# Optimization experiments

Hardware: AMD Instinct MI355X
Metric: run time of the kernel (lower is better)

The kernel has to match this reference:

```python
import jax, jax.numpy as jnp
import numpy as np

WINDOW_SIZE = 2
SOFTMAX_TEMP = 0.01
EPS = 1e-12  # F.normalize default eps


def _l2_normalize(x, axis):
    n = jnp.sqrt(jnp.sum(x * x, axis=axis, keepdims=True))
    return x / jnp.maximum(n, EPS)


def setup_inputs() -> dict:
    key = jax.random.key(0)
    k1, k2, k3 = jax.random.split(key, 3)
    B, C, N = 16, 128, 4096
    return {
        "keypoint_coords": jax.random.normal(k1, (B, 2, N), dtype=jnp.float32),
        "keypoint_weights": jax.random.uniform(k2, (B, 1, N), dtype=jnp.float32),
        "keypoint_desc": jax.random.normal(k3, (B, C, N), dtype=jnp.float32),
    }


def reference(keypoint_coords, keypoint_weights, keypoint_desc):
    # split interleaved src/tgt frames along batch
    src_coords = keypoint_coords[::WINDOW_SIZE]    # [b,2,N]
    tgt_coords = keypoint_coords[1::WINDOW_SIZE]   # [b,2,M]
    src_weights = keypoint_weights[::WINDOW_SIZE]  # [b,1,N]
    tgt_weights = keypoint_weights[1::WINDOW_SIZE] # [b,1,M]
    src_desc = keypoint_desc[::WINDOW_SIZE]        # [b,C,N]
    tgt_desc = keypoint_desc[1::WINDOW_SIZE]       # [b,C,M]

    C = src_desc.shape[1]
    src_desc_norm = _l2_normalize(src_desc, axis=1)
    tgt_desc_norm = _l2_normalize(tgt_desc, axis=1)

    # cosine similarity matrix [b,N,M]
    match_vals = jnp.einsum("bcn,bcm->bnm", src_desc_norm, tgt_desc_norm)
    soft_match_vals = jax.nn.softmax(match_vals / SOFTMAX_TEMP, axis=2)

    # reuse the attention matrix for three value matmuls
    pseudo_coords = jnp.einsum("bcm,bnm->bcn", tgt_coords, soft_match_vals)   # [b,2,N]
    pseudo_desc = jnp.einsum("bcm,bnm->bcn", tgt_desc, soft_match_vals)       # [b,C,N]
    pseudo_desc = _l2_normalize(pseudo_desc, axis=1)
    pseudo_weights = jnp.einsum("bim,bnm->bin", tgt_weights, soft_match_vals) # [b,1,N]

    desc_match_score = jnp.sum(src_desc * pseudo_desc, axis=1, keepdims=True) / float(C)
    match_weights = 0.5 * (desc_match_score + 1.0) * src_weights * pseudo_weights
    return pseudo_coords, match_weights
```

## Files before the change

kernel.cpp:

```cpp
#include <hip/hip_runtime.h>
#include <math.h>

#define C 128
#define N 4096
#define BP 8
#define TN 64

typedef __attribute__((ext_vector_type(8))) short bf16x8;
typedef __attribute__((ext_vector_type(16))) float f32x16;
typedef __attribute__((ext_vector_type(4))) int i32x4;
typedef __attribute__((ext_vector_type(16))) int i32x16;

#define PREP_OFF 65536
#define FRAGS_PER_MT 18
#define SUBT_BYTES (FRAGS_PER_MT * 1024)
#define BLOB_BYTES ((size_t)BP * 128 * FRAGS_PER_MT * 1024)

__device__ __forceinline__ unsigned short bf16rnd(float x) {
  unsigned u = __float_as_uint(x);
  u += 0x7fffu + ((u >> 16) & 1u);
  return (unsigned short)(u >> 16);
}
__device__ __forceinline__ float bf16up(unsigned short h) {
  return __uint_as_float(((unsigned)h) << 16);
}
__device__ __forceinline__ int rne2(float x, float y) {
  unsigned ux = __float_as_uint(x); ux += 0x7fffu + ((ux >> 16) & 1u);
  unsigned uy = __float_as_uint(y); uy += 0x7fffu + ((uy >> 16) & 1u);
  return (int)__builtin_amdgcn_perm(uy, ux, 0x07060302u);
}
__device__ __forceinline__ int trunc2(float x, float y) {
  return (int)__builtin_amdgcn_perm(__float_as_uint(y), __float_as_uint(x), 0x07060302u);
}
__device__ __forceinline__ float truncres(float x) {
  return x - __uint_as_float(__float_as_uint(x) & 0xffff0000u);
}
__device__ __forceinline__ int pk4(int a, int b, int c, int d) {
  return (a & 255) | ((b & 255) << 8) | ((c & 255) << 16) | ((d & 255) << 24);
}

__global__ __launch_bounds__(256) void knorm_inv(const float* __restrict__ desc,
                                                 float* __restrict__ inv) {
  int n = blockIdx.x * 256 + threadIdx.x;
  int b = 2 * blockIdx.y + 1;
  const float* d = desc + (size_t)b * C * N + n;
  float ssq = 0.f;
#pragma unroll 8
  for (int c = 0; c < C; ++c) {
    float v = d[(size_t)c * N];
    ssq = fmaf(v, v, ssq);
  }
  inv[b * N + n] = 1.0f / fmaxf(sqrtf(ssq), 1e-12f);
}

__global__ __launch_bounds__(256) void kprep(
    const float* __restrict__ coords, const float* __restrict__ wtsp,
    const float* __restrict__ desc, unsigned char* __restrict__ blob) {
  const int mt = blockIdx.x;
  const int p = blockIdx.y;
  const int tb = 2 * p + 1;
  const int m0 = mt * 32;
  const int t = threadIdx.x;
  const int ks = t >> 6;
  const int h = (t >> 5) & 1;
  const int l31 = t & 31;

  __shared__ float rss[8][32];

  const float* tgtd = desc + (size_t)tb * C * N;
  unsigned char* bl = blob + ((size_t)(p * 128 + mt) * FRAGS_PER_MT) * 1024;

  float vr[16];
  float part = 0.f;
#pragma unroll
  for (int i = 0; i < 16; ++i) {
    float v = tgtd[(size_t)(32 * ks + 16 * h + i) * N + m0 + l31];
    vr[i] = v;
    part = fmaf(v, v, part);
  }
  rss[ks * 2 + h][l31] = part;
  __syncthreads();
  float ssq = 0.f;
#pragma unroll
  for (int u = 0; u < 8; ++u) ssq += rss[u][l31];
  const float invm = 1.0f / fmaxf(sqrtf(ssq), 1e-12f);

  {
    int hb[16], lb[16];
#pragma unroll
    for (int i = 0; i < 16; ++i) {
      int q = (int)rintf(vr[i] * invm * 16384.f);
      int hi = (q + 128) >> 8;
      hb[i] = hi;
      lb[i] = q - (hi << 8);
    }
    int4 ph = make_int4(pk4(hb[0], hb[1], hb[2], hb[3]), pk4(hb[4], hb[5], hb[6], hb[7]),
                        pk4(hb[8], hb[9], hb[10], hb[11]), pk4(hb[12], hb[13], hb[14], hb[15]));
    int4 pl = make_int4(pk4(lb[0], lb[1], lb[2], lb[3]), pk4(lb[4], lb[5], lb[6], lb[7]),
                        pk4(lb[8], lb[9], lb[10], lb[11]), pk4(lb[12], lb[13], lb[14], lb[15]));
    int lane = 32 * h + l31;
    *(int4*)(bl + (size_t)ks * 1024 + lane * 16) = ph;
    *(int4*)(bl + (size_t)(4 + ks) * 1024 + lane * 16) = pl;
  }

#pragma unroll
  for (int it = 0; it < 4; ++it) {
    int e = t + 256 * it;
    int c = e >> 3, mq = e & 7;
    float4 v = *(const float4*)&tgtd[(size_t)c * N + m0 + 4 * mq];
    int f = (c >> 5) * 2 + (mq >> 2);
    int slot = (c & 31) + 32 * ((mq >> 1) & 1);
    int2 pk;
    pk.x = rne2(v.x, v.y);
    pk.y = rne2(v.z, v.w);
    *(int2*)(bl + (size_t)(8 + f) * 1024 + slot * 16 + (mq & 1) * 8) = pk;
  }

  if (t < 128) {
    int fe = t >> 6, slot = t & 63, r = slot & 31, hh = slot >> 5;
    int4 pk = make_int4(0, 0, 0, 0);
    if (r < 4) {
      const float* rp = (r == 0)   ? coords + (size_t)tb * 2 * N
                        : (r == 1) ? coords + (size_t)tb * 2 * N + N
                                   : wtsp + (size_t)tb * N;
      int mb = m0 + 16 * fe + 8 * hh;
      float v[8];
#pragma unroll
      for (int i = 0; i < 8; ++i) v[i] = (r == 3) ? 1.0f : rp[mb + i];
      pk.x = rne2(v[0], v[1]);
      pk.y = rne2(v[2], v[3]);
      pk.z = rne2(v[4], v[5]);
      pk.w = rne2(v[6], v[7]);
    }
    *(int4*)(bl + (size_t)(16 + fe) * 1024 + slot * 16) = pk;
  }
}

#define LDS_SHORTS 32768

__global__ __launch_bounds__(256, 2) void kmain(
    const float* __restrict__ wtsp, const float* __restrict__ desc,
    const unsigned char* __restrict__ blob, float* __restrict__ out) {
  const int bid = blockIdx.x;
  const int p = bid & 7;
  const int ntile = bid >> 3;
  const int sb = 2 * p;
  const int n0 = ntile * TN;
  const int tid = threadIdx.x;
  const int w = tid >> 6;
  const int ln = tid & 63;
  const int l31 = ln & 31;
  const int h = ln >> 5;
  const int wn = w & 1;
  const int st = w >> 1;

  __shared__ __align__(16) short L[LDS_SHORTS];

  const float* srcd = desc + (size_t)sb * C * N;
  const unsigned char* wblob = blob + (size_t)p * 128 * SUBT_BYTES;
  const int nn = n0 + 32 * wn + l31;

  float ssq = 0.f;
#pragma unroll
  for (int ks = 0; ks < 4; ++ks) {
#pragma unroll
    for (int i = 0; i < 16; ++i) {
      float v = srcd[(size_t)(32 * ks + 16 * h + i) * N + nn];
      ssq = fmaf(v, v, ssq);
    }
  }
  ssq += __shfl_xor(ssq, 32);
  const float invs = 1.0f / fmaxf(sqrtf(ssq), 1e-12f);

  i32x4 Qhi[4], Qlo[4];
#pragma unroll
  for (int ks = 0; ks < 4; ++ks) {
    int hb[16], lb[16];
#pragma unroll
    for (int i = 0; i < 16; ++i) {
      float v = srcd[(size_t)(32 * ks + 16 * h + i) * N + nn] * invs;
      int q = (int)rintf(v * 16384.f);
      int hi = (q + 128) >> 8;
      hb[i] = hi;
      lb[i] = q - (hi << 8);
    }
    i32x4 qh = {pk4(hb[0], hb[1], hb[2], hb[3]), pk4(hb[4], hb[5], hb[6], hb[7]),
                pk4(hb[8], hb[9], hb[10], hb[11]), pk4(hb[12], hb[13], hb[14], hb[15])};
    i32x4 ql = {pk4(lb[0], lb[1], lb[2], lb[3]), pk4(lb[4], lb[5], lb[6], lb[7]),
                pk4(lb[8], lb[9], lb[10], lb[11]), pk4(lb[12], lb[13], lb[14], lb[15])};
    Qhi[ks] = qh;
    Qlo[ks] = ql;
  }

  f32x16 acc[5];
#pragma unroll
  for (int t = 0; t < 5; ++t)
#pragma unroll
    for (int r = 0; r < 16; ++r) acc[t][r] = 0.f;

  i32x16 zz;
#pragma unroll
  for (int r = 0; r < 16; ++r) zz[r] = 0;

  auto issue_dma = [&](int it) {
    const unsigned char* s0 = wblob + (size_t)(it * 2) * SUBT_BYTES + ln * 16;
    short* dst = &L[(it & 3) * 8192];
#pragma unroll
    for (int jj = 0; jj < 4; ++jj) {
      int jg = 4 * w + jj;
      const unsigned char* src = s0 + (size_t)(jg >> 3) * SUBT_BYTES + (size_t)(jg & 7) * 1024;
      __builtin_amdgcn_global_load_lds(
          (const void __attribute__((address_space(1)))*)src,
          (void __attribute__((address_space(3)))*)&dst[jg * 512], 16, 0, 0);
    }
  };
  auto loadV = [&](int it2, int s2, bf16x8* V) {
    const unsigned char* vb =
        wblob + (size_t)(it2 * 2 + st) * SUBT_BYTES + (size_t)(8 + s2) * 1024 + ln * 16;
#pragma unroll
    for (int t = 0; t < 5; ++t) V[t] = *(const bf16x8*)(vb + (size_t)(2 * t) * 1024);
  };

  bf16x8 V0[5], V1[5];

  auto compute_iter = [&](int it) {
    const short* vb = &L[(it & 3) * 8192 + st * 4096];

    i32x16 Shh, Sx, Sll;
    {
      i32x4 ah = *(const i32x4*)&vb[0 * 512 + ln * 8];
      i32x4 al = *(const i32x4*)&vb[4 * 512 + ln * 8];
      Shh = __builtin_amdgcn_mfma_i32_32x32x32_i8(ah, Qhi[0], zz, 0, 0, 0);
      Sx = __builtin_amdgcn_mfma_i32_32x32x32_i8(ah, Qlo[0], zz, 0, 0, 0);
      Sll = __builtin_amdgcn_mfma_i32_32x32x32_i8(al, Qlo[0], zz, 0, 0, 0);
      Sx = __builtin_amdgcn_mfma_i32_32x32x32_i8(al, Qhi[0], Sx, 0, 0, 0);
    }
#pragma unroll
    for (int ks = 1; ks < 4; ++ks) {
      i32x4 ah = *(const i32x4*)&vb[ks * 512 + ln * 8];
      i32x4 al = *(const i32x4*)&vb[(4 + ks) * 512 + ln * 8];
      Shh = __builtin_amdgcn_mfma_i32_32x32x32_i8(ah, Qhi[ks], Shh, 0, 0, 0);
      Sx = __builtin_amdgcn_mfma_i32_32x32x32_i8(ah, Qlo[ks], Sx, 0, 0, 0);
      Sll = __builtin_amdgcn_mfma_i32_32x32x32_i8(al, Qlo[ks], Sll, 0, 0, 0);
      Sx = __builtin_amdgcn_mfma_i32_32x32x32_i8(al, Qhi[ks], Sx, 0, 0, 0);
    }

    loadV(it, 1, V1);

    int pp[8], xpp[8];
#pragma unroll
    for (int q = 0; q < 4; ++q) {
      float pv[4];
#pragma unroll
      for (int j = 0; j < 4; ++j) {
        int r = 4 * q + j;
        int tot = (Shh[r] << 8) + Sx[r];
        float sf = fmaf((float)tot, 256.f, (float)Sll[r]);
        pv[j] = __expf(fmaf(sf, 3.7252903e-07f, -60.0f));
      }
      pp[2 * q] = rne2(pv[0], pv[1]);
      pp[2 * q + 1] = rne2(pv[2], pv[3]);
    }
#pragma unroll
    for (int j = 0; j < 8; ++j) xpp[j] = __shfl_xor(pp[j], 32);

    {
      int4 bi;
      if (h == 0)
        bi = make_int4(pp[0], pp[1], xpp[0], xpp[1]);
      else
        bi = make_int4(xpp[2], xpp[3], pp[2], pp[3]);
      bf16x8 bh = __builtin_bit_cast(bf16x8, bi);
#pragma unroll
      for (int t = 0; t < 5; ++t)
        acc[t] = __builtin_amdgcn_mfma_f32_32x32x16_bf16(V0[t], bh, acc[t], 0, 0, 0);
    }

    {
      int itn = (it < 63) ? it + 1 : 63;
      loadV(itn, 0, V0);
    }

    {
      int4 bi;
      if (h == 0)
        bi = make_int4(pp[4], pp[5], xpp[4], xpp[5]);
      else
        bi = make_int4(xpp[6], xpp[7], pp[6], pp[7]);
      bf16x8 bh = __builtin_bit_cast(bf16x8, bi);
#pragma unroll
      for (int t = 0; t < 5; ++t)
        acc[t] = __builtin_amdgcn_mfma_f32_32x32x16_bf16(V1[t], bh, acc[t], 0, 0, 0);
    }
  };

  issue_dma(0);
  issue_dma(1);
  loadV(0, 0, V0);
  __syncthreads();

  for (int it2 = 0; it2 < 32; ++it2) {
    if (it2 < 31) {
      issue_dma(2 * it2 + 2);
      issue_dma(2 * it2 + 3);
    }
    compute_iter(2 * it2);
    compute_iter(2 * it2 + 1);
    __syncthreads();
  }

  float* red = (float*)&L[0];
  if (st == 1) {
#pragma unroll
    for (int t = 0; t < 5; ++t)
#pragma unroll
      for (int r = 0; r < 16; ++r)
        red[wn * 5120 + t * 1024 + r * 64 + ln] = acc[t][r];
  }
  __syncthreads();

  if (st == 0) {
#pragma unroll
    for (int t = 0; t < 5; ++t)
#pragma unroll
      for (int r = 0; r < 16; ++r)
        acc[t][r] += red[wn * 5120 + t * 1024 + r * 64 + ln];

    float ssqd = 0.f, dotr = 0.f;
#pragma unroll
    for (int t = 0; t < 4; ++t) {
#pragma unroll
      for (int r = 0; r < 16; ++r) {
        int c = 32 * t + (r & 3) + 8 * (r >> 2) + 4 * h;
        float d = acc[t][r];
        ssqd = fmaf(d, d, ssqd);
        dotr = fmaf(d, srcd[(size_t)c * N + nn], dotr);
      }
    }
    ssqd += __shfl_xor(ssqd, 32);
    dotr += __shfl_xor(dotr, 32);
    if (h == 0) {
      float x = acc[4][0], y = acc[4][1], wv = acc[4][2], Ld = acc[4][3];
      float invL = 1.0f / Ld;
      float nrm = fmaxf(sqrtf(ssqd), 1e-30f);
      float score = dotr / (nrm * 128.0f);
      float sw = wtsp[(size_t)sb * N + nn];
      out[(size_t)p * 2 * N + nn] = x * invL;
      out[(size_t)p * 2 * N + N + nn] = y * invL;
      out[(size_t)(BP * 2 * N) + (size_t)p * N + nn] =
          0.5f * (score + 1.0f) * sw * wv * invL;
    }
  }
}

#define OFF_VMH3 0
#define OFF_VML3 8192
#define OFF_VCM3 16384
#define OFF_PH3 26624
#define LDS3_SHORTS 30720

__global__ __launch_bounds__(256, 2) void kmain_v3(
    const float* __restrict__ coords, const float* __restrict__ wtsp,
    const float* __restrict__ desc, const float* __restrict__ inv,
    float* __restrict__ out) {
  const int ntile = blockIdx.x;
  const int p = blockIdx.y;
  const int sb = 2 * p, tb = 2 * p + 1;
  const int n0 = ntile * TN;
  const int tid = threadIdx.x;
  const int w = tid >> 6;
  const int ln = tid & 63;
  const int l31 = ln & 31;
  const int h = ln >> 5;
  const int wn = w & 1;
  const int st = w >> 1;
  const int pt = wn * 64 + ln;

  __shared__ __align__(16) short L[LDS3_SHORTS];

  const float* srcd = desc + (size_t)sb * C * N;
  const float* tgtd = desc + (size_t)tb * C * N;
  const float* invtg = inv + tb * N;
  const float* tcx = coords + (size_t)tb * 2 * N;
  const float* tcy = tcx + N;
  const float* twp = wtsp + (size_t)tb * N;
  const int nn = n0 + 32 * wn + l31;

  float ssq = 0.f;
#pragma unroll
  for (int k = 0; k < 8; ++k) {
    int cb = 16 * k + 8 * h;
#pragma unroll
    for (int i = 0; i < 8; ++i) {
      float v = srcd[(size_t)(cb + i) * N + nn];
      ssq = fmaf(v, v, ssq);
    }
  }
  ssq += __shfl_xor(ssq, 32);
  float invs = 1.0f / fmaxf(sqrtf(ssq), 1e-12f);

  bf16x8 Qh[8], Ql[8];
#pragma unroll
  for (int k = 0; k < 8; ++k) {
    int cb = 16 * k + 8 * h;
    bf16x8 qh, ql;
#pragma unroll
    for (int i = 0; i < 8; ++i) {
      float v = srcd[(size_t)(cb + i) * N + nn] * invs;
      unsigned short hs = bf16rnd(v);
      unsigned short ls = bf16rnd(v - bf16up(hs));
      qh[i] = (short)hs;
      ql[i] = (short)ls;
    }
    Qh[k] = qh;
    Ql[k] = ql;
  }

  {
    int* z = (int*)&L[OFF_VCM3];
    for (int i = tid; i < 1024; i += 256) {
      int sI = i >> 9, j = i & 511;
      z[sI * 2560 + 2048 + j] = 0;
    }
  }

  f32x16 acc[5];
#pragma unroll
  for (int t = 0; t < 5; ++t)
#pragma unroll
    for (int r = 0; r < 16; ++r) acc[t][r] = 0.f;

  const int er = pt & 3, ehh = (pt >> 2) & 1, esf = pt >> 3;
  const float* erp = (er == 0) ? tcx : (er == 1) ? tcy : twp;

  float vm[32];
  float invm = 0.f;
  float4 exv0 = make_float4(1, 1, 1, 1), exv1 = exv0;

  auto prefetch = [&](int ms0) {
#pragma unroll
    for (int k = 0; k < 4; ++k) {
      int cb = 16 * (2 * k + wn) + 8 * h;
#pragma unroll
      for (int i = 0; i < 8; ++i)
        vm[k * 8 + i] = tgtd[(size_t)(cb + i) * N + ms0 + l31];
    }
    invm = invtg[ms0 + l31];
    if (pt < 16 && er < 3) {
      int mb = ms0 + 16 * esf + 8 * ehh;
      exv0 = *(const float4*)&erp[mb];
      exv1 = *(const float4*)&erp[mb + 4];
    }
  };

  prefetch(32 * st);

  for (int m0 = 0; m0 < N; m0 += 64) {
    const int ms0 = m0 + 32 * st;
    float4 vc[8];
#pragma unroll
    for (int it = 0; it < 8; ++it) {
      int e = pt + 128 * it, c = e >> 3, mq = e & 7;
      vc[it] = *(const float4*)&tgtd[(size_t)c * N + ms0 + 4 * mq];
    }
#pragma unroll
    for (int k = 0; k < 4; ++k) {
      int kk = 2 * k + wn;
      int hw[4], lw[4];
#pragma unroll
      for (int j = 0; j < 4; ++j) {
        float v0 = vm[k * 8 + 2 * j] * invm;
        float v1 = vm[k * 8 + 2 * j + 1] * invm;
        hw[j] = trunc2(v0, v1);
        lw[j] = trunc2(truncres(v0), truncres(v1));
      }
      *(int4*)&L[OFF_VMH3 + st * 4096 + kk * 512 + ln * 8] =
          make_int4(hw[0], hw[1], hw[2], hw[3]);
      *(int4*)&L[OFF_VML3 + st * 4096 + kk * 512 + ln * 8] =
          make_int4(lw[0], lw[1], lw[2], lw[3]);
    }
#pragma unroll
    for (int it = 0; it < 8; ++it) {
      int e = pt + 128 * it, c = e >> 3, mq = e & 7;
      float4 v = vc[it];
      int f = (c >> 5) * 2 + (mq >> 2);
      int slot = (c & 31) + 32 * ((mq >> 1) & 1);
      int2 pk;
      pk.x = rne2(v.x, v.y);
      pk.y = rne2(v.z, v.w);
      *(int2*)&L[OFF_VCM3 + st * 5120 + f * 512 + slot * 8 + (mq & 1) * 4] = pk;
    }
    if (pt < 16) {
      int4 pk;
      pk.x = rne2(exv0.x, exv0.y);
      pk.y = rne2(exv0.z, exv0.w);
      pk.z = rne2(exv1.x, exv1.y);
      pk.w = rne2(exv1.z, exv1.w);
      *(int4*)&L[OFF_VCM3 + st * 5120 + (8 + esf) * 512 + (er + 32 * ehh) * 8] = pk;
    }
    __syncthreads();
    if (m0 + 64 < N) prefetch(ms0 + 64);

    f32x16 S;
#pragma unroll
    for (int r = 0; r < 16; ++r) S[r] = 0.f;
    const short* vmh = &L[OFF_VMH3 + st * 4096];
    const short* vml = &L[OFF_VML3 + st * 4096];
#pragma unroll
    for (int k = 0; k < 8; ++k) {
      bf16x8 ah = *(const bf16x8*)&vmh[k * 512 + ln * 8];
      bf16x8 al = *(const bf16x8*)&vml[k * 512 + ln * 8];
      S = __builtin_amdgcn_mfma_f32_32x32x16_bf16(al, Qh[k], S, 0, 0, 0);
      S = __builtin_amdgcn_mfma_f32_32x32x16_bf16(ah, Ql[k], S, 0, 0, 0);
      S = __builtin_amdgcn_mfma_f32_32x32x16_bf16(ah, Qh[k], S, 0, 0, 0);
    }
#pragma unroll
    for (int q = 0; q < 4; ++q) {
      float p0 = __expf(fmaf(S[4 * q + 0], 100.0f, -60.0f));
      float p1 = __expf(fmaf(S[4 * q + 1], 100.0f, -60.0f));
      float p2 = __expf(fmaf(S[4 * q + 2], 100.0f, -60.0f));
      float p3 = __expf(fmaf(S[4 * q + 3], 100.0f, -60.0f));
      int2 a;
      a.x = rne2(p0, p1);
      a.y = rne2(p2, p3);
      *(int2*)&L[OFF_PH3 + w * 1024 + (q >> 1) * 512 + (l31 + 32 * (q & 1)) * 8 + h * 4] = a;
    }
#pragma unroll
    for (int s2 = 0; s2 < 2; ++s2) {
      bf16x8 bh = *(const bf16x8*)&L[OFF_PH3 + w * 1024 + s2 * 512 + ln * 8];
#pragma unroll
      for (int t = 0; t < 5; ++t) {
        bf16x8 va = *(const bf16x8*)&L[OFF_VCM3 + st * 5120 + (2 * t + s2) * 512 + ln * 8];
        acc[t] = __builtin_amdgcn_mfma_f32_32x32x16_bf16(va, bh, acc[t], 0, 0, 0);
      }
    }
    __syncthreads();
  }

  float* red = (float*)&L[0];
  if (st == 1) {
#pragma unroll
    for (int t = 0; t < 5; ++t)
#pragma unroll
      for (int r = 0; r < 16; ++r)
        red[wn * 5120 + t * 1024 + r * 64 + ln] = acc[t][r];
  }
  __syncthreads();
  if (st == 0) {
#pragma unroll
    for (int t = 0; t < 5; ++t)
#pragma unroll
      for (int r = 0; r < 16; ++r)
        acc[t][r] += red[wn * 5120 + t * 1024 + r * 64 + ln];
    float ssqd = 0.f, dotr = 0.f;
#pragma unroll
    for (int t = 0; t < 4; ++t) {
#pragma unroll
      for (int r = 0; r < 16; ++r) {
        int c = 32 * t + (r & 3) + 8 * (r >> 2) + 4 * h;
        float d = acc[t][r];
        ssqd = fmaf(d, d, ssqd);
        dotr = fmaf(d, srcd[(size_t)c * N + nn], dotr);
      }
    }
    ssqd += __shfl_xor(ssqd, 32);
    dotr += __shfl_xor(dotr, 32);
    if (h == 0) {
      float x = acc[4][0], y = acc[4][1], wv = acc[4][2], Ld = acc[4][3];
      float invL = 1.0f / Ld;
      float nrm = fmaxf(sqrtf(ssqd), 1e-30f);
      float score = dotr / (nrm * 128.0f);
      float sw = wtsp[(size_t)sb * N + nn];
      out[(size_t)p * 2 * N + nn] = x * invL;
      out[(size_t)p * 2 * N + N + nn] = y * invL;
      out[(size_t)(BP * 2 * N) + (size_t)p * N + nn] =
          0.5f * (score + 1.0f) * sw * wv * invL;
    }
  }
}

extern "C" void kernel_launch(void* const* d_in, const int* in_sizes, int n_in,
                              void* d_out, int out_size, void* d_ws, size_t ws_size,
                              hipStream_t stream) {
  const float* coords = (const float*)d_in[0];
  const float* wts = (const float*)d_in[1];
  const float* desc = (const float*)d_in[2];
  float* out = (float*)d_out;
  float* inv = (float*)d_ws;
  unsigned char* blob = (unsigned char*)d_ws + PREP_OFF;

  if (ws_size >= PREP_OFF + BLOB_BYTES) {
    kprep<<<dim3(128, BP), 256, 0, stream>>>(coords, wts, desc, blob);
    kmain<<<dim3((N / TN) * BP), 256, 0, stream>>>(wts, desc, blob, out);
  } else {
    knorm_inv<<<dim3(N / 256, BP), 256, 0, stream>>>(desc, inv);
    kmain_v3<<<dim3(N / TN, BP), 256, 0, stream>>>(coords, wts, desc, inv, out);
  }
}
```

Baseline: 203.4 us.

## Give each wave a private LDS double buffer and drop per-iteration block barriers

Each wave now DMAs its own K sub-tile fragments into a private double-buffered LDS region and waits only on its own outstanding loads with s_waitcnt, instead of cooperatively loading a shared quad-buffered tile and hitting __syncthreads every two iterations. This removes block-wide barrier stalls from the main loop. It also rewrites the exp as exp2 with a pre-scaled constant. The trade-off is duplicated global traffic when several waves need the same fragments, and a correctness dependence on the waitcnt immediate being right.

```diff
diff --git a/kernel.cpp b/kernel.cpp
--- a/kernel.cpp
+++ b/kernel.cpp
@@ -203,15 +203,14 @@
   for (int r = 0; r < 16; ++r) zz[r] = 0;
 
   auto issue_dma = [&](int it) {
-    const unsigned char* s0 = wblob + (size_t)(it * 2) * SUBT_BYTES + ln * 16;
-    short* dst = &L[(it & 3) * 8192];
-#pragma unroll
-    for (int jj = 0; jj < 4; ++jj) {
-      int jg = 4 * w + jj;
-      const unsigned char* src = s0 + (size_t)(jg >> 3) * SUBT_BYTES + (size_t)(jg & 7) * 1024;
+    const unsigned char* s0 =
+        wblob + (size_t)(it * 2 + st) * SUBT_BYTES + ln * 16;
+    short* dst = &L[w * 8192 + (it & 1) * 4096];
+#pragma unroll
+    for (int f = 0; f < 8; ++f) {
       __builtin_amdgcn_global_load_lds(
-          (const void __attribute__((address_space(1)))*)src,
-          (void __attribute__((address_space(3)))*)&dst[jg * 512], 16, 0, 0);
+          (const void __attribute__((address_space(1)))*)(s0 + (size_t)f * 1024),
+          (void __attribute__((address_space(3)))*)&dst[f * 512], 16, 0, 0);
     }
   };
   auto loadV = [&](int it2, int s2, bf16x8* V) {
@@ -223,8 +222,14 @@
 
   bf16x8 V0[5], V1[5];
 
-  auto compute_iter = [&](int it) {
-    const short* vb = &L[(it & 3) * 8192 + st * 4096];
+  issue_dma(0);
+  loadV(0, 0, V0);
+
+  for (int it = 0; it < 64; ++it) {
+    if (it < 63) issue_dma(it + 1);
+    __builtin_amdgcn_s_waitcnt(0x0F78);
+
+    const short* vb = &L[w * 8192 + (it & 1) * 4096];
 
     i32x16 Shh, Sx, Sll;
     {
@@ -256,7 +261,7 @@
         int r = 4 * q + j;
         int tot = (Shh[r] << 8) + Sx[r];
         float sf = fmaf((float)tot, 256.f, (float)Sll[r]);
-        pv[j] = __expf(fmaf(sf, 3.7252903e-07f, -60.0f));
+        pv[j] = exp2f(fmaf(sf, 5.3744005e-07f, -86.561646f));
       }
       pp[2 * q] = rne2(pv[0], pv[1]);
       pp[2 * q + 1] = rne2(pv[2], pv[3]);
@@ -292,23 +297,9 @@
       for (int t = 0; t < 5; ++t)
         acc[t] = __builtin_amdgcn_mfma_f32_32x32x16_bf16(V1[t], bh, acc[t], 0, 0, 0);
     }
-  };
-
-  issue_dma(0);
-  issue_dma(1);
-  loadV(0, 0, V0);
+  }
+
   __syncthreads();
-
-  for (int it2 = 0; it2 < 32; ++it2) {
-    if (it2 < 31) {
-      issue_dma(2 * it2 + 2);
-      issue_dma(2 * it2 + 3);
-    }
-    compute_iter(2 * it2);
-    compute_iter(2 * it2 + 1);
-    __syncthreads();
-  }
-
   float* red = (float*)&L[0];
   if (st == 1) {
 #pragma unroll
```

Result: slower. 221.5 us (+8.9%).

## Software-pipeline PV matmul of previous tile with QK matmul of current tile

Applied to the files above, without the earlier changes.

Restructures the inner loop so the P·V MFMAs for the previous key tile are interleaved with the int8 QK MFMAs of the current tile. The exp/pack step now runs separately and stores packed probabilities in carried registers, with a drain step after the loop. This is meant to hide the dependency stall between QK, exp and PV and keep the matrix units busy. The exponential also switches from __expf to exp2f with constants pre-multiplied by log2(e). The cost is more live registers (all ten V fragments plus the carried P fragments) and an extra epilogue.

```diff
diff --git a/kernel.cpp b/kernel.cpp
--- a/kernel.cpp
+++ b/kernel.cpp
@@ -214,19 +214,27 @@
           (void __attribute__((address_space(3)))*)&dst[jg * 512], 16, 0, 0);
     }
   };
-  auto loadV = [&](int it2, int s2, bf16x8* V) {
+  auto loadV = [&](int it2, bf16x8* V) {
     const unsigned char* vb =
-        wblob + (size_t)(it2 * 2 + st) * SUBT_BYTES + (size_t)(8 + s2) * 1024 + ln * 16;
-#pragma unroll
-    for (int t = 0; t < 5; ++t) V[t] = *(const bf16x8*)(vb + (size_t)(2 * t) * 1024);
+        wblob + (size_t)(it2 * 2 + st) * SUBT_BYTES + (size_t)8 * 1024 + ln * 16;
+#pragma unroll
+    for (int s2 = 0; s2 < 2; ++s2)
+#pragma unroll
+      for (int t = 0; t < 5; ++t)
+        V[s2 * 5 + t] = *(const bf16x8*)(vb + (size_t)(2 * t + s2) * 1024);
   };
 
-  bf16x8 V0[5], V1[5];
-
-  auto compute_iter = [&](int it) {
+  int4 PF0 = make_int4(0, 0, 0, 0), PF1 = make_int4(0, 0, 0, 0);
+  bf16x8 Vp[10];
+#pragma unroll
+  for (int k = 0; k < 10; ++k) Vp[k] = __builtin_bit_cast(bf16x8, make_int4(0, 0, 0, 0));
+
+  i32x16 Shh, Sx, Sll;
+
+  auto qk_pv = [&](int it) {
     const short* vb = &L[(it & 3) * 8192 + st * 4096];
-
-    i32x16 Shh, Sx, Sll;
+    bf16x8 bh0 = __builtin_bit_cast(bf16x8, PF0);
+    bf16x8 bh1 = __builtin_bit_cast(bf16x8, PF1);
     {
       i32x4 ah = *(const i32x4*)&vb[0 * 512 + ln * 8];
       i32x4 al = *(const i32x4*)&vb[4 * 512 + ln * 8];
@@ -234,19 +242,44 @@
       Sx = __builtin_amdgcn_mfma_i32_32x32x32_i8(ah, Qlo[0], zz, 0, 0, 0);
       Sll = __builtin_amdgcn_mfma_i32_32x32x32_i8(al, Qlo[0], zz, 0, 0, 0);
       Sx = __builtin_amdgcn_mfma_i32_32x32x32_i8(al, Qhi[0], Sx, 0, 0, 0);
-    }
-#pragma unroll
-    for (int ks = 1; ks < 4; ++ks) {
-      i32x4 ah = *(const i32x4*)&vb[ks * 512 + ln * 8];
-      i32x4 al = *(const i32x4*)&vb[(4 + ks) * 512 + ln * 8];
-      Shh = __builtin_amdgcn_mfma_i32_32x32x32_i8(ah, Qhi[ks], Shh, 0, 0, 0);
-      Sx = __builtin_amdgcn_mfma_i32_32x32x32_i8(ah, Qlo[ks], Sx, 0, 0, 0);
-      Sll = __builtin_amdgcn_mfma_i32_32x32x32_i8(al, Qlo[ks], Sll, 0, 0, 0);
-      Sx = __builtin_amdgcn_mfma_i32_32x32x32_i8(al, Qhi[ks], Sx, 0, 0, 0);
-    }
-
-    loadV(it, 1, V1);
-
+      acc[0] = __builtin_amdgcn_mfma_f32_32x32x16_bf16(Vp[0], bh0, acc[0], 0, 0, 0);
+      acc[1] = __builtin_amdgcn_mfma_f32_32x32x16_bf16(Vp[1], bh0, acc[1], 0, 0, 0);
+      acc[2] = __builtin_amdgcn_mfma_f32_32x32x16_bf16(Vp[2], bh0, acc[2], 0, 0, 0);
+    }
+    {
+      i32x4 ah = *(const i32x4*)&vb[1 * 512 + ln * 8];
+      i32x4 al = *(const i32x4*)&vb[5 * 512 + ln * 8];
+      Shh = __builtin_amdgcn_mfma_i32_32x32x32_i8(ah, Qhi[1], Shh, 0, 0, 0);
+      Sx = __builtin_amdgcn_mfma_i32_32x32x32_i8(ah, Qlo[1], Sx, 0, 0, 0);
+      Sll = __builtin_amdgcn_mfma_i32_32x32x32_i8(al, Qlo[1], Sll, 0, 0, 0);
+      Sx = __builtin_amdgcn_mfma_i32_32x32x32_i8(al, Qhi[1], Sx, 0, 0, 0);
+      acc[3] = __builtin_amdgcn_mfma_f32_32x32x16_bf16(Vp[3], bh0, acc[3], 0, 0, 0);
+      acc[4] = __builtin_amdgcn_mfma_f32_32x32x16_bf16(Vp[4], bh0, acc[4], 0, 0, 0);
+    }
+    {
+      i32x4 ah = *(const i32x4*)&vb[2 * 512 + ln * 8];
+      i32x4 al = *(const i32x4*)&vb[6 * 512 + ln * 8];
+      Shh = __builtin_amdgcn_mfma_i32_32x32x32_i8(ah, Qhi[2], Shh, 0, 0, 0);
+      Sx = __builtin_amdgcn_mfma_i32_32x32x32_i8(ah, Qlo[2], Sx, 0, 0, 0);
+      Sll = __builtin_amdgcn_mfma_i32_32x32x32_i8(al, Qlo[2], Sll, 0, 0, 0);
+      Sx = __builtin_amdgcn_mfma_i32_32x32x32_i8(al, Qhi[2], Sx, 0, 0, 0);
+      acc[0] = __builtin_amdgcn_mfma_f32_32x32x16_bf16(Vp[5], bh1, acc[0], 0, 0, 0);
+      acc[1] = __builtin_amdgcn_mfma_f32_32x32x16_bf16(Vp[6], bh1, acc[1], 0, 0, 0);
+      acc[2] = __builtin_amdgcn_mfma_f32_32x32x16_bf16(Vp[7], bh1, acc[2], 0, 0, 0);
+    }
+    {
+      i32x4 ah = *(const i32x4*)&vb[3 * 512 + ln * 8];
+      i32x4 al = *(const i32x4*)&vb[7 * 512 + ln * 8];
+      Shh = __builtin_amdgcn_mfma_i32_32x32x32_i8(ah, Qhi[3], Shh, 0, 0, 0);
+      Sx = __builtin_amdgcn_mfma_i32_32x32x32_i8(ah, Qlo[3], Sx, 0, 0, 0);
+      Sll = __builtin_amdgcn_mfma_i32_32x32x32_i8(al, Qlo[3], Sll, 0, 0, 0);
+      Sx = __builtin_amdgcn_mfma_i32_32x32x32_i8(al, Qhi[3], Sx, 0, 0, 0);
+      acc[3] = __builtin_amdgcn_mfma_f32_32x32x16_bf16(Vp[8], bh1, acc[3], 0, 0, 0);
+      acc[4] = __builtin_amdgcn_mfma_f32_32x32x16_bf16(Vp[9], bh1, acc[4], 0, 0, 0);
+    }
+  };
+
+  auto exp_pack = [&]() {
     int pp[8], xpp[8];
 #pragma unroll
     for (int q = 0; q < 4; ++q) {
@@ -256,57 +289,49 @@
         int r = 4 * q + j;
         int tot = (Shh[r] << 8) + Sx[r];
         float sf = fmaf((float)tot, 256.f, (float)Sll[r]);
-        pv[j] = __expf(fmaf(sf, 3.7252903e-07f, -60.0f));
+        pv[j] = exp2f(fmaf(sf, 5.3744005e-07f, -86.561646f));
       }
       pp[2 * q] = rne2(pv[0], pv[1]);
       pp[2 * q + 1] = rne2(pv[2], pv[3]);
     }
 #pragma unroll
     for (int j = 0; j < 8; ++j) xpp[j] = __shfl_xor(pp[j], 32);
-
-    {
-      int4 bi;
-      if (h == 0)
-        bi = make_int4(pp[0], pp[1], xpp[0], xpp[1]);
-      else
-        bi = make_int4(xpp[2], xpp[3], pp[2], pp[3]);
-      bf16x8 bh = __builtin_bit_cast(bf16x8, bi);
-#pragma unroll
-      for (int t = 0; t < 5; ++t)
-        acc[t] = __builtin_amdgcn_mfma_f32_32x32x16_bf16(V0[t], bh, acc[t], 0, 0, 0);
-    }
-
-    {
-      int itn = (it < 63) ? it + 1 : 63;
-      loadV(itn, 0, V0);
-    }
-
-    {
-      int4 bi;
-      if (h == 0)
-        bi = make_int4(pp[4], pp[5], xpp[4], xpp[5]);
-      else
-        bi = make_int4(xpp[6], xpp[7], pp[6], pp[7]);
-      bf16x8 bh = __builtin_bit_cast(bf16x8, bi);
-#pragma unroll
-      for (int t = 0; t < 5; ++t)
-        acc[t] = __builtin_amdgcn_mfma_f32_32x32x16_bf16(V1[t], bh, acc[t], 0, 0, 0);
+    if (h == 0) {
+      PF0 = make_int4(pp[0], pp[1], xpp[0], xpp[1]);
+      PF1 = make_int4(pp[4], pp[5], xpp[4], xpp[5]);
+    } else {
+      PF0 = make_int4(xpp[2], xpp[3], pp[2], pp[3]);
+      PF1 = make_int4(xpp[6], xpp[7], pp[6], pp[7]);
     }
   };
 
   issue_dma(0);
   issue_dma(1);
-  loadV(0, 0, V0);
   __syncthreads();
 
-  for (int it2 = 0; it2 < 32; ++it2) {
-    if (it2 < 31) {
-      issue_dma(2 * it2 + 2);
-      issue_dma(2 * it2 + 3);
-    }
-    compute_iter(2 * it2);
-    compute_iter(2 * it2 + 1);
+  for (int j = 0; j < 32; ++j) {
+    if (j < 31) {
+      issue_dma(2 * j + 2);
+      issue_dma(2 * j + 3);
+    }
+    qk_pv(2 * j);
+    exp_pack();
+    loadV(2 * j, Vp);
+    qk_pv(2 * j + 1);
+    exp_pack();
+    loadV(2 * j + 1, Vp);
     __syncthreads();
+  }
+
+  {
+    bf16x8 bh0 = __builtin_bit_cast(bf16x8, PF0);
+    bf16x8 bh1 = __builtin_bit_cast(bf16x8, PF1);
+#pragma unroll
+    for (int t = 0; t < 5; ++t)
+      acc[t] = __builtin_amdgcn_mfma_f32_32x32x16_bf16(Vp[t], bh0, acc[t], 0, 0, 0);
+#pragma unroll
+    for (int t = 0; t < 5; ++t)
+      acc[t] = __builtin_amdgcn_mfma_f32_32x32x16_bf16(Vp[5 + t], bh1, acc[t], 0, 0, 0);
   }
 
   float* red = (float*)&L[0];
```

Result: no change. 203.0 us (-0.2%).
